# Kernel tuning notes

Hardware: AMD Instinct MI355X
Metric: run time of the kernel (lower is better)

Reference implementation:

```python
import jax, jax.numpy as jnp
import numpy as np

K = 3
STRIDE = 1
PAD = 1
C_IN = 128
C_OUT = 256

def setup_inputs() -> dict:
    key = jax.random.key(0)
    kx, kw, kb = jax.random.split(key, 3)
    x = jax.random.normal(kx, (32, C_IN, 56, 56), dtype=jnp.float32)
    # torch init: uniform(-1/K, 1/K) for kernels, uniform(-1/sqrt(Cout), 1/sqrt(Cout)) for bias
    kernels = jax.random.uniform(kw, (C_OUT, C_IN, K, K), dtype=jnp.float32,
                                 minval=-1.0 / K, maxval=1.0 / K)
    b = jax.random.uniform(kb, (C_OUT,), dtype=jnp.float32,
                           minval=-1.0 / C_OUT ** 0.5, maxval=1.0 / C_OUT ** 0.5)
    return {"x": x, "kernels": kernels, "b": b}

def reference(x, kernels, b):
    # Same math as the im2col broadcast-matmul + channel-sum: a standard 2D conv
    # with zero padding, expressed as one contracted GEMM via conv_general_dilated.
    out = jax.lax.conv_general_dilated(
        x, kernels,
        window_strides=(STRIDE, STRIDE),
        padding=((PAD, PAD), (PAD, PAD)),
        dimension_numbers=("NCHW", "OIHW", "NCHW"),
    )
    return out + b.reshape(1, C_OUT, 1, 1)
```

## Files before the change

### kernel.cpp

```cpp
#include <hip/hip_runtime.h>
#include <hip/hip_bf16.h>

#define NB   32
#define CIN  128
#define COUT 256
#define HH   56
#define WW   56
#define CH   59

typedef __attribute__((ext_vector_type(8))) short short8;
typedef __attribute__((ext_vector_type(4))) float f32x4;

__device__ __forceinline__ unsigned short f2bf(float f) {
    unsigned int u = __builtin_bit_cast(unsigned int, f);
    u = u + 0x7fffu + ((u >> 16) & 1u);
    return (unsigned short)(u >> 16);
}

__global__ __launch_bounds__(256) void wpose_kernel(const float* __restrict__ w,
                                                    unsigned short* __restrict__ wt2) {
    int q = blockIdx.x * 256 + threadIdx.x;
    if (q >= 36 * 16 * 64 * 8) return;
    int j = q & 7;
    int l = (q >> 3) & 63;
    int f = (q >> 9) & 15;
    int s = q >> 13;
    int g = l >> 4, r = l & 15;
    int t = s >> 2, cc = s & 3;
    int o = f * 16 + r;
    int c = cc * 32 + g * 8 + j;
    wt2[q] = f2bf(w[((size_t)o * CIN + c) * 9 + t]);
}

__global__ __launch_bounds__(256, 2) void conv_mfma_kernel(
        const float* __restrict__ x,
        const unsigned short* __restrict__ wt2,
        const float* __restrict__ bias,
        float* __restrict__ out) {
    __shared__ unsigned short ldsB[4 * 16 * CH * 8];

    const int tid  = threadIdx.x;
    const int h0   = blockIdx.x * 2, n = blockIdx.y;
    const int wm   = tid >> 6, lane = tid & 63;
    const int g    = lane >> 4, r = lane & 15;

    for (int i = tid; i < 4 * 16 * CH; i += 256) {
        uint4 z = {0u, 0u, 0u, 0u};
        *(uint4*)&ldsB[(size_t)i * 8] = z;
    }
    __syncthreads();

    {
        const float* xn = x + (size_t)n * CIN * HH * WW;
        for (int i = tid; i < 4 * 64 * 14; i += 256) {
            int w4  = i % 14;
            int t1  = i / 14;
            int cp  = t1 & 63;
            int row = t1 >> 6;
            int hs  = h0 + row - 1;
            if ((unsigned)hs < HH) {
                const float* p = xn + ((size_t)(2 * cp) * HH + hs) * WW + 4 * w4;
                float4 va = *(const float4*)p;
                float4 vb = *(const float4*)(p + HH * WW);
                int gc = cp >> 2, e = cp & 3;
                #pragma unroll
                for (int j = 0; j < 4; ++j) {
                    int wpos = 4 * w4 + j + 1;
                    unsigned int pk = (unsigned int)f2bf(((const float*)&va)[j])
                                    | ((unsigned int)f2bf(((const float*)&vb)[j]) << 16);
                    ((unsigned int*)ldsB)[((row * 16 + gc) * CH + wpos) * 4 + e] = pk;
                }
            }
        }
    }
    __syncthreads();

    const unsigned short* bbase[7];
    int hrv[7];
    #pragma unroll
    for (int ni = 0; ni < 7; ++ni) {
        int c  = ni * 16 + r;
        int hr = (c >= 56) ? 1 : 0;
        hrv[ni] = hr;
        int lo = hr * (16 * CH) + (c - hr * 56);
        bbase[ni] = &ldsB[(size_t)(g * CH + lo) * 8];
    }

    f32x4 acc[4][7];
    #pragma unroll
    for (int mi = 0; mi < 4; ++mi)
        #pragma unroll
        for (int ni = 0; ni < 7; ++ni)
            #pragma unroll
            for (int v = 0; v < 4; ++v) acc[mi][ni][v] = 0.f;

    const short8* abase = (const short8*)wt2 + (size_t)(wm * 4) * 64 + lane;

    #pragma unroll
    for (int t = 0; t < 9; ++t) {
        const int kh = t / 3, kw = t - 3 * (t / 3);
        #pragma unroll
        for (int cc = 0; cc < 4; ++cc) {
            const int s = t * 4 + cc;
            const int boff = kh * 15104 + cc * 3776 + kw * 16;

            short8 a[4];
            #pragma unroll
            for (int mi = 0; mi < 4; ++mi)
                a[mi] = abase[(size_t)s * 1024 + mi * 64];

            short8 b[7];
            #pragma unroll
            for (int ni = 0; ni < 7; ++ni)
                b[ni] = *(const short8*)((const char*)bbase[ni] + boff);

            #pragma unroll
            for (int mi = 0; mi < 4; ++mi)
                #pragma unroll
                for (int ni = 0; ni < 7; ++ni)
                    acc[mi][ni] = __builtin_amdgcn_mfma_f32_16x16x32_bf16(
                        a[mi], b[ni], acc[mi][ni], 0, 0, 0);
        }
    }

    #pragma unroll
    for (int mi = 0; mi < 4; ++mi) {
        const int o0 = wm * 64 + mi * 16 + 4 * g;
        const float4 bv = *(const float4*)&bias[o0];
        #pragma unroll
        for (int ni = 0; ni < 7; ++ni) {
            const int c = ni * 16 + r;
            const int h = h0 + hrv[ni];
            const int w = c - hrv[ni] * 56;
            #pragma unroll
            for (int v = 0; v < 4; ++v) {
                out[((size_t)(n * COUT + o0 + v) * HH + h) * WW + w] =
                    acc[mi][ni][v] + ((const float*)&bv)[v];
            }
        }
    }
}

extern "C" void kernel_launch(void* const* d_in, const int* in_sizes, int n_in,
                              void* d_out, int out_size, void* d_ws, size_t ws_size,
                              hipStream_t stream) {
    const float* x  = (const float*)d_in[0];
    const float* wk = (const float*)d_in[1];
    const float* b  = (const float*)d_in[2];
    float* out = (float*)d_out;

    unsigned short* wt2 = (unsigned short*)d_ws;

    wpose_kernel<<<(36 * 16 * 64 * 8 + 255) / 256, 256, 0, stream>>>(wk, wt2);
    dim3 gc(28, NB);
    conv_mfma_kernel<<<gc, 256, 0, stream>>>(x, wt2, b, out);
    (void)ws_size; (void)in_sizes; (void)n_in; (void)out_size;
}
```

Baseline: 81.02 us.

## Widen conv block to four output rows and double-buffer weights via global_load_lds

Each block now computes four output rows with 512 threads split into two N-groups of 4 waves, so each weight tile is reused across more spatial positions and the input halo overhead drops (6 staged rows for 4 outputs instead of 4 for 2). Weight fragments are no longer read straight from global memory. They are prefetched per wave into a double-buffered LDS region with async global_load_lds and gated by vmcnt waits. This adds LDS use (about 113KB+64KB per block), which may cap occupancy at one block per CU and halves the grid to 448 blocks. The waitcnt handling assumes no other outstanding vector loads.

```diff
diff --git a/kernel.cpp b/kernel.cpp
--- a/kernel.cpp
+++ b/kernel.cpp
@@ -17,6 +17,13 @@
     return (unsigned short)(u >> 16);
 }
 
+__device__ __forceinline__ void glds16(const unsigned short* g, unsigned short* l) {
+    __builtin_amdgcn_global_load_lds(
+        (const __attribute__((address_space(1))) unsigned int*)g,
+        (__attribute__((address_space(3))) unsigned int*)l,
+        16, 0, 0);
+}
+
 __global__ __launch_bounds__(256) void wpose_kernel(const float* __restrict__ w,
                                                     unsigned short* __restrict__ wt2) {
     int q = blockIdx.x * 256 + threadIdx.x;
@@ -32,19 +39,21 @@
     wt2[q] = f2bf(w[((size_t)o * CIN + c) * 9 + t]);
 }
 
-__global__ __launch_bounds__(256, 2) void conv_mfma_kernel(
+__global__ __launch_bounds__(512, 2) void conv_mfma_kernel(
         const float* __restrict__ x,
         const unsigned short* __restrict__ wt2,
         const float* __restrict__ bias,
         float* __restrict__ out) {
-    __shared__ unsigned short ldsB[4 * 16 * CH * 8];
+    __shared__ unsigned short ldsB[6 * 16 * CH * 8];
+    __shared__ unsigned short ldsA[8 * 2 * 2048];
 
     const int tid  = threadIdx.x;
-    const int h0   = blockIdx.x * 2, n = blockIdx.y;
-    const int wm   = tid >> 6, lane = tid & 63;
+    const int h0   = blockIdx.x * 4, n = blockIdx.y;
+    const int wid  = tid >> 6, lane = tid & 63;
+    const int wm   = wid >> 1, wn = wid & 1;
     const int g    = lane >> 4, r = lane & 15;
 
-    for (int i = tid; i < 4 * 16 * CH; i += 256) {
+    for (int i = tid; i < 6 * 16 * CH; i += 512) {
         uint4 z = {0u, 0u, 0u, 0u};
         *(uint4*)&ldsB[(size_t)i * 8] = z;
     }
@@ -52,7 +61,7 @@
 
     {
         const float* xn = x + (size_t)n * CIN * HH * WW;
-        for (int i = tid; i < 4 * 64 * 14; i += 256) {
+        for (int i = tid; i < 6 * 64 * 14; i += 512) {
             int w4  = i % 14;
             int t1  = i / 14;
             int cp  = t1 & 63;
@@ -73,17 +82,29 @@
             }
         }
     }
+
+    unsigned short* aslot = &ldsA[(size_t)wid * 2 * 2048];
+    #define STAGE_A(slot, s)                                                    \
+        {                                                                       \
+            const unsigned short* asrc_ =                                       \
+                wt2 + ((size_t)(s) * 16 + wm * 4) * 512 + lane * 8;             \
+            unsigned short* adst_ = aslot + (slot) * 2048;                      \
+            glds16(asrc_,        adst_);                                        \
+            glds16(asrc_ + 512,  adst_ + 512);                                  \
+            glds16(asrc_ + 1024, adst_ + 1024);                                 \
+            glds16(asrc_ + 1536, adst_ + 1536);                                 \
+        }
+
+    STAGE_A(0, 0);
     __syncthreads();
 
     const unsigned short* bbase[7];
-    int hrv[7];
     #pragma unroll
     for (int ni = 0; ni < 7; ++ni) {
         int c  = ni * 16 + r;
         int hr = (c >= 56) ? 1 : 0;
-        hrv[ni] = hr;
         int lo = hr * (16 * CH) + (c - hr * 56);
-        bbase[ni] = &ldsB[(size_t)(g * CH + lo) * 8];
+        bbase[ni] = &ldsB[(size_t)((wn * 32 + g) * CH + lo) * 8];
     }
 
     f32x4 acc[4][7];
@@ -94,7 +115,7 @@
             #pragma unroll
             for (int v = 0; v < 4; ++v) acc[mi][ni][v] = 0.f;
 
-    const short8* abase = (const short8*)wt2 + (size_t)(wm * 4) * 64 + lane;
+    const unsigned short* aread = aslot + lane * 8;
 
     #pragma unroll
     for (int t = 0; t < 9; ++t) {
@@ -102,12 +123,18 @@
         #pragma unroll
         for (int cc = 0; cc < 4; ++cc) {
             const int s = t * 4 + cc;
+            const int p = s & 1;
             const int boff = kh * 15104 + cc * 3776 + kw * 16;
+
+            if (s < 35) STAGE_A(p ^ 1, s + 1);
+
+            if (s < 35) asm volatile("s_waitcnt vmcnt(4)" ::: "memory");
+            else        asm volatile("s_waitcnt vmcnt(0)" ::: "memory");
 
             short8 a[4];
             #pragma unroll
             for (int mi = 0; mi < 4; ++mi)
-                a[mi] = abase[(size_t)s * 1024 + mi * 64];
+                a[mi] = *(const short8*)(aread + p * 2048 + mi * 512);
 
             short8 b[7];
             #pragma unroll
@@ -129,9 +156,10 @@
         const float4 bv = *(const float4*)&bias[o0];
         #pragma unroll
         for (int ni = 0; ni < 7; ++ni) {
-            const int c = ni * 16 + r;
-            const int h = h0 + hrv[ni];
-            const int w = c - hrv[ni] * 56;
+            const int c  = ni * 16 + r;
+            const int hr = (c >= 56) ? 1 : 0;
+            const int h  = h0 + wn * 2 + hr;
+            const int w  = c - hr * 56;
             #pragma unroll
             for (int v = 0; v < 4; ++v) {
                 out[((size_t)(n * COUT + o0 + v) * HH + h) * WW + w] =
@@ -152,7 +180,7 @@
     unsigned short* wt2 = (unsigned short*)d_ws;
 
     wpose_kernel<<<(36 * 16 * 64 * 8 + 255) / 256, 256, 0, stream>>>(wk, wt2);
-    dim3 gc(28, NB);
-    conv_mfma_kernel<<<gc, 256, 0, stream>>>(x, wt2, b, out);
+    dim3 gc(14, NB);
+    conv_mfma_kernel<<<gc, 512, 0, stream>>>(x, wt2, b, out);
     (void)ws_size; (void)in_sizes; (void)n_in; (void)out_size;
 }
```

Result: faster. 73.44 us (-9.3%).
